# Kernel optimization log

Hardware: AMD Instinct MI355X
Metric: run time of the kernel (lower is better)

## Reference

```python
import jax, jax.numpy as jnp
import numpy as np

EPS = 1e-6


def setup_inputs() -> dict:
    key = jax.random.key(0)
    kq, kk, kv = jax.random.split(key, 3)
    B, H, S, D = 1, 16, 2048, 64
    q = jax.random.normal(kq, (B, H, S, D), dtype=jnp.float32)
    k = jax.random.normal(kk, (B, H, S, D), dtype=jnp.float32)
    v = jax.random.normal(kv, (B, H, S, D), dtype=jnp.float32)
    return {"q": q, "k": k, "v": v}


def reference(q, k, v):
    # Rebased linear attention: squared scaled QK score, causal mask,
    # normalized by running row-sum (not softmax).
    B, H, S, D = q.shape
    scale = D ** (-0.5)
    # [B,H,S,S] raw scores
    s = jnp.einsum("bhid,bhjd->bhij", q, k) * scale
    s2 = s * s
    causal = jnp.tril(jnp.ones((S, S), dtype=bool))  # k_idx <= q_idx
    s2 = jnp.where(causal, s2, jnp.zeros((), dtype=s2.dtype))
    z = jnp.sum(s2, axis=-1)  # [B,H,S]
    o = jnp.einsum("bhij,bhjd->bhid", s2, v)
    return o / (z[..., None] + EPS)
```

## Files before the change

### kernel.cpp

```cpp
#include <hip/hip_runtime.h>

typedef __attribute__((ext_vector_type(8))) short bf16x8;
typedef __attribute__((ext_vector_type(16))) float f32x16;

#define SLEN 2048
#define DDIM 64
#define NH 16
#define KEPS 1e-6f
#define TILE_B 16384
#define PSTR 72

__device__ __forceinline__ short f2bf(float x) {
    unsigned u = __float_as_uint(x);
    unsigned r = (u + 0x7FFFu + ((u >> 16) & 1u)) >> 16;
    return (short)r;
}
__device__ __forceinline__ unsigned cvtpk(float lo, float hi) {
    unsigned r;
    asm("v_cvt_pk_bf16_f32 %0, %1, %2" : "=v"(r) : "v"(lo), "v"(hi));
    return r;
}
__device__ __forceinline__ f32x16 mfma32x32(bf16x8 a, bf16x8 b, f32x16 c) {
    return __builtin_amdgcn_mfma_f32_32x32x16_bf16(a, b, c, 0, 0, 0);
}
__device__ __forceinline__ void gload16(const void* g, void* l) {
    __builtin_amdgcn_global_load_lds(
        (const __attribute__((address_space(1))) unsigned*)g,
        (__attribute__((address_space(3))) unsigned*)l, 16, 0, 0);
}

__global__ void __launch_bounds__(256) prep_kernel(
    const float* __restrict__ K, const float* __restrict__ V, char* __restrict__ WS)
{
    __shared__ short vt[64 * PSTR];
    const int b  = blockIdx.x;
    const int h  = b >> 5;
    const int kt = b & 31;
    const int t  = threadIdx.x;
    const int j  = t >> 2;
    const int ks = t & 3;
    const int c16 = ks * 16;

    char* chunk = WS + (size_t)b * TILE_B;

    {
        const float* src = K + ((size_t)h * SLEN + kt * 64 + j) * DDIM + c16;
        float4 a = ((const float4*)src)[0], bb = ((const float4*)src)[1];
        float4 c = ((const float4*)src)[2], d = ((const float4*)src)[3];
        uint4 lo = make_uint4(cvtpk(a.x,a.y), cvtpk(a.z,a.w), cvtpk(bb.x,bb.y), cvtpk(bb.z,bb.w));
        uint4 hi = make_uint4(cvtpk(c.x,c.y), cvtpk(c.z,c.w), cvtpk(d.x,d.y), cvtpk(d.z,d.w));
        *(uint4*)(chunk + ((size_t)((ks*2+0)*64 + j)) * 16) = lo;
        *(uint4*)(chunk + ((size_t)((ks*2+1)*64 + j)) * 16) = hi;
    }
    {
        const float* src = V + ((size_t)h * SLEN + kt * 64 + j) * DDIM + c16;
        float4 a = ((const float4*)src)[0], bb = ((const float4*)src)[1];
        float4 c = ((const float4*)src)[2], d = ((const float4*)src)[3];
        float f[16] = {a.x,a.y,a.z,a.w, bb.x,bb.y,bb.z,bb.w, c.x,c.y,c.z,c.w, d.x,d.y,d.z,d.w};
#pragma unroll
        for (int q = 0; q < 16; ++q)
            vt[(c16 + q) * PSTR + j] = f2bf(f[q]);
    }
    __syncthreads();
    {
        const int d  = t >> 2;
        const int jc = (t & 3) * 16;
        uint4 lo = *(const uint4*)&vt[d * PSTR + jc];
        uint4 hi = *(const uint4*)&vt[d * PSTR + jc + 8];
        char* vbase = chunk + 8192;
        *(uint4*)(vbase + (size_t)(((jc >> 4) * 2 + 0) * 64 + d) * 16) = lo;
        *(uint4*)(vbase + (size_t)(((jc >> 4) * 2 + 1) * 64 + d) * 16) = hi;
    }
}

template<bool WSP>
__device__ __forceinline__ void attn_body(
    const float* __restrict__ Q, const void* __restrict__ s1,
    const void* __restrict__ s2, float* __restrict__ O)
{
    __shared__ __align__(16) char smem[2][2][TILE_B];

    const int bid   = blockIdx.x;
    const int xcd   = bid & 7;
    const int r     = bid >> 3;
    const int h     = xcd | ((r & 1) << 3);
    const int u     = r >> 1;
    const int pg    = u & 15;
    const int halfb = u >> 4;

    const int tid  = threadIdx.x;
    const int w    = tid >> 6;
    const int lane = tid & 63;
    const int il   = lane & 31;
    const int hi   = lane >> 5;
    const int p    = w >> 2;
    const int qsel = (w >> 1) & 1;
    const int jb   = w & 1;

    const int grp   = qsel ? (31 - pg) : pg;
    const int q0    = grp * 64 + halfb * 32;
    const int ktmax = grp;
    const int ktstg = 31 - pg;

    const float* __restrict__ Qh = Q + (size_t)h * SLEN * DDIM;
    float* __restrict__ Oh = O + (size_t)h * SLEN * DDIM;

    bf16x8 qf[4];
#pragma unroll
    for (int ks = 0; ks < 4; ++ks) {
        const float* src = Qh + (size_t)(q0 + il) * DDIM + ks * 16 + hi * 8;
        float4 a = *reinterpret_cast<const float4*>(src);
        float4 b = *reinterpret_cast<const float4*>(src + 4);
        uint4 uq = make_uint4(cvtpk(a.x, a.y), cvtpk(a.z, a.w),
                              cvtpk(b.x, b.y), cvtpk(b.z, b.w));
        qf[ks] = *reinterpret_cast<bf16x8*>(&uq);
    }

    f32x16 oacc0, oacc1;
#pragma unroll
    for (int rr = 0; rr < 16; ++rr) { oacc0[rr] = 0.f; oacc1[rr] = 0.f; }
    float zacc = 0.f;

    const int wv = w & 3;
    const char* WSh = (const char*)s1 + (size_t)h * 32 * TILE_B;
    const int t255 = tid & 255;
    const int kr = t255 >> 2, kks = t255 & 3;
    const int vj0 = (t255 & 15) * 4, vd0 = (t255 >> 4) * 4;
    const float* Kf = (const float*)s1;
    const float* Vf = (const float*)s2;
    float4 kv[4], vv[4];

    auto stage_async = [&](int buf, int kt) {
        const char* g = WSh + (size_t)kt * TILE_B + wv * 4096 + lane * 16;
        char* l = &smem[p][buf][wv * 4096];
        gload16(g,        l);
        gload16(g + 1024, l + 1024);
        gload16(g + 2048, l + 2048);
        gload16(g + 3072, l + 3072);
    };
    auto issue_loads = [&](int kt) {
        const float* ks = Kf + ((size_t)h * SLEN + kt * 64 + kr) * DDIM + kks * 16;
#pragma unroll
        for (int i = 0; i < 4; ++i) kv[i] = reinterpret_cast<const float4*>(ks)[i];
#pragma unroll
        for (int rr = 0; rr < 4; ++rr)
            vv[rr] = *reinterpret_cast<const float4*>(
                Vf + ((size_t)h * SLEN + kt * 64 + vj0 + rr) * DDIM + vd0);
    };
    auto write_lds = [&](int buf) {
        char* kd = &smem[p][buf][0];
        uint4 lo = make_uint4(cvtpk(kv[0].x,kv[0].y), cvtpk(kv[0].z,kv[0].w),
                              cvtpk(kv[1].x,kv[1].y), cvtpk(kv[1].z,kv[1].w));
        uint4 hii = make_uint4(cvtpk(kv[2].x,kv[2].y), cvtpk(kv[2].z,kv[2].w),
                               cvtpk(kv[3].x,kv[3].y), cvtpk(kv[3].z,kv[3].w));
        *(uint4*)(kd + (size_t)((kks*2+0)*64 + kr) * 16) = lo;
        *(uint4*)(kd + (size_t)((kks*2+1)*64 + kr) * 16) = hii;
        char* vd = &smem[p][buf][8192];
        const int cv  = ((vj0 >> 4) * 2) + ((vj0 >> 3) & 1);
        const int tof = vj0 & 7;
#pragma unroll
        for (int c = 0; c < 4; ++c) {
            uint2 pk = make_uint2(
                cvtpk(((const float*)&vv[0])[c], ((const float*)&vv[1])[c]),
                cvtpk(((const float*)&vv[2])[c], ((const float*)&vv[3])[c]));
            *(uint2*)(vd + (size_t)(cv * 64 + vd0 + c) * 16 + tof * 2) = pk;
        }
    };

    const int T = (ktstg >> 1) + 1;

    if (WSP) { stage_async(0, p); }
    else     { issue_loads(p); write_lds(0); }
    __syncthreads();

    for (int t = 0; t < T; ++t) {
        const int kt  = 2 * t + p;
        const int nxt = kt + 2;
        const int cur = t & 1;

        if (nxt <= ktstg) { if (WSP) stage_async(cur ^ 1, nxt); else issue_loads(nxt); }

        if (kt <= ktmax && !(kt == ktmax && jb > halfb)) {
            const bool tri = (kt == ktmax) && (jb == halfb);
            const short* kp = (const short*)&smem[p][cur][0];
            const short* vp = (const short*)&smem[p][cur][8192];
            __builtin_amdgcn_s_setprio(1);
            f32x16 s;
#pragma unroll
            for (int rr = 0; rr < 16; ++rr) s[rr] = 0.f;
#pragma unroll
            for (int ks = 0; ks < 4; ++ks) {
                bf16x8 kf = *reinterpret_cast<const bf16x8*>(
                    kp + (size_t)((ks*2+hi)*64 + jb*32 + il) * 8);
                s = mfma32x32(kf, qf[ks], s);
            }
#pragma unroll
            for (int rr = 0; rr < 16; ++rr) {
                float x = s[rr];
                x = x * x * 0.015625f;
                if (tri) {
                    int jl = (rr & 3) + 8 * (rr >> 2) + 4 * hi;
                    if (jl > il) x = 0.f;
                }
                s[rr] = x;
                zacc += x;
            }
#pragma unroll
            for (int s16 = 0; s16 < 2; ++s16) {
                unsigned X  = cvtpk(s[8*s16+0], s[8*s16+1]);
                unsigned Xp = cvtpk(s[8*s16+2], s[8*s16+3]);
                unsigned Y  = cvtpk(s[8*s16+4], s[8*s16+5]);
                unsigned Yp = cvtpk(s[8*s16+6], s[8*s16+7]);
                asm("v_permlane32_swap_b32 %0, %1" : "+v"(X), "+v"(Y));
                asm("v_permlane32_swap_b32 %0, %1" : "+v"(Xp), "+v"(Yp));
                uint4 aw = make_uint4(X, Xp, Y, Yp);
                bf16x8 pf = *reinterpret_cast<bf16x8*>(&aw);
                {
                    bf16x8 vf = *reinterpret_cast<const bf16x8*>(
                        vp + (size_t)(((jb*2+s16)*2+hi)*64 + 0*32 + il) * 8);
                    oacc0 = mfma32x32(pf, vf, oacc0);
                }
                {
                    bf16x8 vf = *reinterpret_cast<const bf16x8*>(
                        vp + (size_t)(((jb*2+s16)*2+hi)*64 + 1*32 + il) * 8);
                    oacc1 = mfma32x32(pf, vf, oacc1);
                }
            }
            __builtin_amdgcn_s_setprio(0);
        }

        if (!WSP && nxt <= ktstg) write_lds(cur ^ 1);
        __syncthreads();
    }

    zacc += __shfl_xor(zacc, 32);
    float* red = (float*)smem;
    const int slot = p * 2 + jb;
    if (slot != 0) {
        float* rr_ = red + (size_t)((((slot - 1) * 2 + qsel) * 64 + lane) * 33);
#pragma unroll
        for (int rr = 0; rr < 16; ++rr) { rr_[rr] = oacc0[rr]; rr_[16 + rr] = oacc1[rr]; }
        rr_[32] = zacc;
    }
    __syncthreads();
    if (slot == 0) {
#pragma unroll
        for (int pp = 1; pp < 4; ++pp) {
            const float* rr_ = red + (size_t)((((pp - 1) * 2 + qsel) * 64 + lane) * 33);
#pragma unroll
            for (int rr = 0; rr < 16; ++rr) { oacc0[rr] += rr_[rr]; oacc1[rr] += rr_[16 + rr]; }
            zacc += rr_[32];
        }
        const float invl = 1.f / (zacc + KEPS);
#pragma unroll
        for (int rr = 0; rr < 16; ++rr) {
            const int rl = (rr & 3) + 8 * (rr >> 2) + 4 * hi;
            const float inv = __shfl(invl, rl);
            Oh[(size_t)(q0 + rl) * DDIM + il]      = oacc0[rr] * inv;
            Oh[(size_t)(q0 + rl) * DDIM + 32 + il] = oacc1[rr] * inv;
        }
    }
}

__global__ void __launch_bounds__(512, 4) attn_ws(
    const float* __restrict__ Q, const char* __restrict__ WS, float* __restrict__ O)
{
    attn_body<true>(Q, WS, nullptr, O);
}
__global__ void __launch_bounds__(512, 4) attn_fp32(
    const float* __restrict__ Q, const float* __restrict__ K,
    const float* __restrict__ V, float* __restrict__ O)
{
    attn_body<false>(Q, K, V, O);
}

extern "C" void kernel_launch(void* const* d_in, const int* in_sizes, int n_in,
                              void* d_out, int out_size, void* d_ws, size_t ws_size,
                              hipStream_t stream) {
    const float* q = (const float*)d_in[0];
    const float* k = (const float*)d_in[1];
    const float* v = (const float*)d_in[2];
    float* o = (float*)d_out;

    const size_t need = (size_t)NH * 32 * TILE_B;
    if (ws_size >= need) {
        char* ws = (char*)d_ws;
        hipLaunchKernelGGL(prep_kernel, dim3(NH * 32), dim3(256), 0, stream, k, v, ws);
        hipLaunchKernelGGL(attn_ws, dim3(512), dim3(512), 0, stream, q, ws, o);
    } else {
        hipLaunchKernelGGL(attn_fp32, dim3(512), dim3(512), 0, stream, q, k, v, o);
    }
}
```

Baseline: 35.75 us.

## Drop LDS staging; load prepacked K/V fragments directly from global into registers

The attention kernel no longer stages K/V tiles through double-buffered shared memory with async global-to-LDS loads and per-iteration barriers. Each wave now reads its MFMA operand fragments straight from the pre-swizzled workspace, prefetching the next K fragments in registers. Work is split so each wave owns one 32-query half, one key sub-block and alternating key tiles, with a reduction across four waves at the end. This removes the barriers and LDS traffic, but relies on L2/cache reuse because several waves re-read the same tiles from global memory.

```diff
diff --git a/kernel.cpp b/kernel.cpp
--- a/kernel.cpp
+++ b/kernel.cpp
@@ -22,11 +22,6 @@
 }
 __device__ __forceinline__ f32x16 mfma32x32(bf16x8 a, bf16x8 b, f32x16 c) {
     return __builtin_amdgcn_mfma_f32_32x32x16_bf16(a, b, c, 0, 0, 0);
-}
-__device__ __forceinline__ void gload16(const void* g, void* l) {
-    __builtin_amdgcn_global_load_lds(
-        (const __attribute__((address_space(1))) unsigned*)g,
-        (__attribute__((address_space(3))) unsigned*)l, 16, 0, 0);
 }
 
 __global__ void __launch_bounds__(256) prep_kernel(
@@ -73,37 +68,33 @@
     }
 }
 
-template<bool WSP>
-__device__ __forceinline__ void attn_body(
-    const float* __restrict__ Q, const void* __restrict__ s1,
-    const void* __restrict__ s2, float* __restrict__ O)
+__global__ void __launch_bounds__(512, 4) attn_main(
+    const float* __restrict__ Q, const char* __restrict__ WS, float* __restrict__ O)
 {
-    __shared__ __align__(16) char smem[2][2][TILE_B];
-
-    const int bid   = blockIdx.x;
-    const int xcd   = bid & 7;
-    const int r     = bid >> 3;
-    const int h     = xcd | ((r & 1) << 3);
-    const int u     = r >> 1;
-    const int pg    = u & 15;
-    const int halfb = u >> 4;
+    __shared__ float red[2][3][64][33];
+
+    const int bid = blockIdx.x;
+    const int xcd = bid & 7;
+    const int m   = bid >> 3;
+    const int h   = xcd | ((m & 1) << 3);
+    const int c   = m >> 1;
 
     const int tid  = threadIdx.x;
     const int w    = tid >> 6;
     const int lane = tid & 63;
     const int il   = lane & 31;
     const int hi   = lane >> 5;
-    const int p    = w >> 2;
-    const int qsel = (w >> 1) & 1;
-    const int jb   = w & 1;
-
-    const int grp   = qsel ? (31 - pg) : pg;
-    const int q0    = grp * 64 + halfb * 32;
-    const int ktmax = grp;
-    const int ktstg = 31 - pg;
+    const int msel = w >> 2;
+    const int jb   = (w >> 1) & 1;
+    const int e    = w & 1;
+
+    const int g    = msel ? (31 - c) : c;
+    const int half = msel;
+    const int q0   = g * 64 + half * 32;
 
     const float* __restrict__ Qh = Q + (size_t)h * SLEN * DDIM;
     float* __restrict__ Oh = O + (size_t)h * SLEN * DDIM;
+    const char* __restrict__ WSh = WS + (size_t)h * 32 * TILE_B;
 
     bf16x8 qf[4];
 #pragma unroll
@@ -121,79 +112,43 @@
     for (int rr = 0; rr < 16; ++rr) { oacc0[rr] = 0.f; oacc1[rr] = 0.f; }
     float zacc = 0.f;
 
-    const int wv = w & 3;
-    const char* WSh = (const char*)s1 + (size_t)h * 32 * TILE_B;
-    const int t255 = tid & 255;
-    const int kr = t255 >> 2, kks = t255 & 3;
-    const int vj0 = (t255 & 15) * 4, vd0 = (t255 >> 4) * 4;
-    const float* Kf = (const float*)s1;
-    const float* Vf = (const float*)s2;
-    float4 kv[4], vv[4];
-
-    auto stage_async = [&](int buf, int kt) {
-        const char* g = WSh + (size_t)kt * TILE_B + wv * 4096 + lane * 16;
-        char* l = &smem[p][buf][wv * 4096];
-        gload16(g,        l);
-        gload16(g + 1024, l + 1024);
-        gload16(g + 2048, l + 2048);
-        gload16(g + 3072, l + 3072);
-    };
-    auto issue_loads = [&](int kt) {
-        const float* ks = Kf + ((size_t)h * SLEN + kt * 64 + kr) * DDIM + kks * 16;
-#pragma unroll
-        for (int i = 0; i < 4; ++i) kv[i] = reinterpret_cast<const float4*>(ks)[i];
-#pragma unroll
-        for (int rr = 0; rr < 4; ++rr)
-            vv[rr] = *reinterpret_cast<const float4*>(
-                Vf + ((size_t)h * SLEN + kt * 64 + vj0 + rr) * DDIM + vd0);
-    };
-    auto write_lds = [&](int buf) {
-        char* kd = &smem[p][buf][0];
-        uint4 lo = make_uint4(cvtpk(kv[0].x,kv[0].y), cvtpk(kv[0].z,kv[0].w),
-                              cvtpk(kv[1].x,kv[1].y), cvtpk(kv[1].z,kv[1].w));
-        uint4 hii = make_uint4(cvtpk(kv[2].x,kv[2].y), cvtpk(kv[2].z,kv[2].w),
-                               cvtpk(kv[3].x,kv[3].y), cvtpk(kv[3].z,kv[3].w));
-        *(uint4*)(kd + (size_t)((kks*2+0)*64 + kr) * 16) = lo;
-        *(uint4*)(kd + (size_t)((kks*2+1)*64 + kr) * 16) = hii;
-        char* vd = &smem[p][buf][8192];
-        const int cv  = ((vj0 >> 4) * 2) + ((vj0 >> 3) & 1);
-        const int tof = vj0 & 7;
-#pragma unroll
-        for (int c = 0; c < 4; ++c) {
-            uint2 pk = make_uint2(
-                cvtpk(((const float*)&vv[0])[c], ((const float*)&vv[1])[c]),
-                cvtpk(((const float*)&vv[2])[c], ((const float*)&vv[3])[c]));
-            *(uint2*)(vd + (size_t)(cv * 64 + vd0 + c) * 16 + tof * 2) = pk;
-        }
-    };
-
-    const int T = (ktstg >> 1) + 1;
-
-    if (WSP) { stage_async(0, p); }
-    else     { issue_loads(p); write_lds(0); }
-    __syncthreads();
-
-    for (int t = 0; t < T; ++t) {
-        const int kt  = 2 * t + p;
-        const int nxt = kt + 2;
-        const int cur = t & 1;
-
-        if (nxt <= ktstg) { if (WSP) stage_async(cur ^ 1, nxt); else issue_loads(nxt); }
-
-        if (kt <= ktmax && !(kt == ktmax && jb > halfb)) {
-            const bool tri = (kt == ktmax) && (jb == halfb);
-            const short* kp = (const short*)&smem[p][cur][0];
-            const short* vp = (const short*)&smem[p][cur][8192];
-            __builtin_amdgcn_s_setprio(1);
+    const int koff = (hi * 64 + jb * 32 + il) * 16;
+    const int voff = 8192 + ((jb * 2 * 2 + hi) * 64 + il) * 16;
+
+    const int ktend = g - ((jb > half) ? 1 : 0);
+
+    if (e <= ktend) {
+        const char* kb = WSh + (size_t)e * TILE_B + koff;
+        bf16x8 kf0 = *(const bf16x8*)(kb);
+        bf16x8 kf1 = *(const bf16x8*)(kb + 2048);
+        bf16x8 kf2 = *(const bf16x8*)(kb + 4096);
+        bf16x8 kf3 = *(const bf16x8*)(kb + 6144);
+
+        for (int kt = e; kt <= ktend; kt += 2) {
+            const char* tb = WSh + (size_t)kt * TILE_B;
+            const char* vb = tb + voff;
+            bf16x8 v00 = *(const bf16x8*)(vb);
+            bf16x8 v01 = *(const bf16x8*)(vb + 512);
+            bf16x8 v10 = *(const bf16x8*)(vb + 2048);
+            bf16x8 v11 = *(const bf16x8*)(vb + 2560);
+
             f32x16 s;
 #pragma unroll
             for (int rr = 0; rr < 16; ++rr) s[rr] = 0.f;
-#pragma unroll
-            for (int ks = 0; ks < 4; ++ks) {
-                bf16x8 kf = *reinterpret_cast<const bf16x8*>(
-                    kp + (size_t)((ks*2+hi)*64 + jb*32 + il) * 8);
-                s = mfma32x32(kf, qf[ks], s);
-            }
+            s = mfma32x32(kf0, qf[0], s);
+            s = mfma32x32(kf1, qf[1], s);
+            s = mfma32x32(kf2, qf[2], s);
+            s = mfma32x32(kf3, qf[3], s);
+
+            if (kt + 2 <= ktend) {
+                const char* nb = WSh + (size_t)(kt + 2) * TILE_B + koff;
+                kf0 = *(const bf16x8*)(nb);
+                kf1 = *(const bf16x8*)(nb + 2048);
+                kf2 = *(const bf16x8*)(nb + 4096);
+                kf3 = *(const bf16x8*)(nb + 6144);
+            }
+
+            const bool tri = (kt == g) && (jb == half);
 #pragma unroll
             for (int rr = 0; rr < 16; ++rr) {
                 float x = s[rr];
@@ -203,53 +158,58 @@
                     if (jl > il) x = 0.f;
                 }
                 s[rr] = x;
-                zacc += x;
-            }
-#pragma unroll
-            for (int s16 = 0; s16 < 2; ++s16) {
-                unsigned X  = cvtpk(s[8*s16+0], s[8*s16+1]);
-                unsigned Xp = cvtpk(s[8*s16+2], s[8*s16+3]);
-                unsigned Y  = cvtpk(s[8*s16+4], s[8*s16+5]);
-                unsigned Yp = cvtpk(s[8*s16+6], s[8*s16+7]);
+            }
+            {
+                float a0 = (s[0] + s[1]) + (s[2] + s[3]);
+                float a1 = (s[4] + s[5]) + (s[6] + s[7]);
+                float a2 = (s[8] + s[9]) + (s[10] + s[11]);
+                float a3 = (s[12] + s[13]) + (s[14] + s[15]);
+                zacc += (a0 + a1) + (a2 + a3);
+            }
+
+            {
+                unsigned X  = cvtpk(s[0], s[1]);
+                unsigned Xp = cvtpk(s[2], s[3]);
+                unsigned Y  = cvtpk(s[4], s[5]);
+                unsigned Yp = cvtpk(s[6], s[7]);
                 asm("v_permlane32_swap_b32 %0, %1" : "+v"(X), "+v"(Y));
                 asm("v_permlane32_swap_b32 %0, %1" : "+v"(Xp), "+v"(Yp));
                 uint4 aw = make_uint4(X, Xp, Y, Yp);
                 bf16x8 pf = *reinterpret_cast<bf16x8*>(&aw);
-                {
-                    bf16x8 vf = *reinterpret_cast<const bf16x8*>(
-                        vp + (size_t)(((jb*2+s16)*2+hi)*64 + 0*32 + il) * 8);
-                    oacc0 = mfma32x32(pf, vf, oacc0);
-                }
-                {
-                    bf16x8 vf = *reinterpret_cast<const bf16x8*>(
-                        vp + (size_t)(((jb*2+s16)*2+hi)*64 + 1*32 + il) * 8);
-                    oacc1 = mfma32x32(pf, vf, oacc1);
-                }
-            }
-            __builtin_amdgcn_s_setprio(0);
-        }
-
-        if (!WSP && nxt <= ktstg) write_lds(cur ^ 1);
-        __syncthreads();
+                oacc0 = mfma32x32(pf, v00, oacc0);
+                oacc1 = mfma32x32(pf, v01, oacc1);
+            }
+            {
+                unsigned X  = cvtpk(s[8],  s[9]);
+                unsigned Xp = cvtpk(s[10], s[11]);
+                unsigned Y  = cvtpk(s[12], s[13]);
+                unsigned Yp = cvtpk(s[14], s[15]);
+                asm("v_permlane32_swap_b32 %0, %1" : "+v"(X), "+v"(Y));
+                asm("v_permlane32_swap_b32 %0, %1" : "+v"(Xp), "+v"(Yp));
+                uint4 aw = make_uint4(X, Xp, Y, Yp);
+                bf16x8 pf = *reinterpret_cast<bf16x8*>(&aw);
+                oacc0 = mfma32x32(pf, v10, oacc0);
+                oacc1 = mfma32x32(pf, v11, oacc1);
+            }
+        }
     }
 
     zacc += __shfl_xor(zacc, 32);
-    float* red = (float*)smem;
-    const int slot = p * 2 + jb;
-    if (slot != 0) {
-        float* rr_ = red + (size_t)((((slot - 1) * 2 + qsel) * 64 + lane) * 33);
-#pragma unroll
-        for (int rr = 0; rr < 16; ++rr) { rr_[rr] = oacc0[rr]; rr_[16 + rr] = oacc1[rr]; }
-        rr_[32] = zacc;
+    const int sw = w & 3;
+    if (sw != 0) {
+        float* r = &red[msel][sw - 1][lane][0];
+#pragma unroll
+        for (int rr = 0; rr < 16; ++rr) { r[rr] = oacc0[rr]; r[16 + rr] = oacc1[rr]; }
+        r[32] = zacc;
     }
     __syncthreads();
-    if (slot == 0) {
-#pragma unroll
-        for (int pp = 1; pp < 4; ++pp) {
-            const float* rr_ = red + (size_t)((((pp - 1) * 2 + qsel) * 64 + lane) * 33);
-#pragma unroll
-            for (int rr = 0; rr < 16; ++rr) { oacc0[rr] += rr_[rr]; oacc1[rr] += rr_[16 + rr]; }
-            zacc += rr_[32];
+    if (sw == 0) {
+#pragma unroll
+        for (int pp = 0; pp < 3; ++pp) {
+            const float* r = &red[msel][pp][lane][0];
+#pragma unroll
+            for (int rr = 0; rr < 16; ++rr) { oacc0[rr] += r[rr]; oacc1[rr] += r[16 + rr]; }
+            zacc += r[32];
         }
         const float invl = 1.f / (zacc + KEPS);
 #pragma unroll
@@ -262,16 +222,130 @@
     }
 }
 
-__global__ void __launch_bounds__(512, 4) attn_ws(
-    const float* __restrict__ Q, const char* __restrict__ WS, float* __restrict__ O)
-{
-    attn_body<true>(Q, WS, nullptr, O);
-}
 __global__ void __launch_bounds__(512, 4) attn_fp32(
     const float* __restrict__ Q, const float* __restrict__ K,
     const float* __restrict__ V, float* __restrict__ O)
 {
-    attn_body<false>(Q, K, V, O);
+    __shared__ float red[2][3][64][33];
+
+    const int bid = blockIdx.x;
+    const int xcd = bid & 7;
+    const int m   = bid >> 3;
+    const int h   = xcd | ((m & 1) << 3);
+    const int c   = m >> 1;
+
+    const int tid  = threadIdx.x;
+    const int w    = tid >> 6;
+    const int lane = tid & 63;
+    const int il   = lane & 31;
+    const int hi   = lane >> 5;
+    const int msel = w >> 2;
+    const int jb   = (w >> 1) & 1;
+    const int e    = w & 1;
+
+    const int g    = msel ? (31 - c) : c;
+    const int half = msel;
+    const int q0   = g * 64 + half * 32;
+
+    const float* Qh = Q + (size_t)h * SLEN * DDIM;
+    const float* Kh = K + (size_t)h * SLEN * DDIM;
+    const float* Vh = V + (size_t)h * SLEN * DDIM;
+    float* Oh = O + (size_t)h * SLEN * DDIM;
+
+    bf16x8 qf[4];
+#pragma unroll
+    for (int ks = 0; ks < 4; ++ks) {
+        const float* src = Qh + (size_t)(q0 + il) * DDIM + ks * 16 + hi * 8;
+        float4 a = *reinterpret_cast<const float4*>(src);
+        float4 b = *reinterpret_cast<const float4*>(src + 4);
+        uint4 uq = make_uint4(cvtpk(a.x, a.y), cvtpk(a.z, a.w),
+                              cvtpk(b.x, b.y), cvtpk(b.z, b.w));
+        qf[ks] = *reinterpret_cast<bf16x8*>(&uq);
+    }
+
+    f32x16 oacc0, oacc1;
+#pragma unroll
+    for (int rr = 0; rr < 16; ++rr) { oacc0[rr] = 0.f; oacc1[rr] = 0.f; }
+    float zacc = 0.f;
+
+    const int ktend = g - ((jb > half) ? 1 : 0);
+
+    for (int kt = e; kt <= ktend; kt += 2) {
+        f32x16 s;
+#pragma unroll
+        for (int rr = 0; rr < 16; ++rr) s[rr] = 0.f;
+#pragma unroll
+        for (int ks = 0; ks < 4; ++ks) {
+            const float* src = Kh + (size_t)(kt * 64 + jb * 32 + il) * DDIM + ks * 16 + hi * 8;
+            float4 a = *reinterpret_cast<const float4*>(src);
+            float4 b = *reinterpret_cast<const float4*>(src + 4);
+            uint4 uk = make_uint4(cvtpk(a.x, a.y), cvtpk(a.z, a.w),
+                                  cvtpk(b.x, b.y), cvtpk(b.z, b.w));
+            s = mfma32x32(*reinterpret_cast<bf16x8*>(&uk), qf[ks], s);
+        }
+        const bool tri = (kt == g) && (jb == half);
+#pragma unroll
+        for (int rr = 0; rr < 16; ++rr) {
+            float x = s[rr];
+            x = x * x * 0.015625f;
+            if (tri) {
+                int jl = (rr & 3) + 8 * (rr >> 2) + 4 * hi;
+                if (jl > il) x = 0.f;
+            }
+            s[rr] = x;
+            zacc += x;
+        }
+#pragma unroll
+        for (int s16 = 0; s16 < 2; ++s16) {
+            unsigned X  = cvtpk(s[8*s16+0], s[8*s16+1]);
+            unsigned Xp = cvtpk(s[8*s16+2], s[8*s16+3]);
+            unsigned Y  = cvtpk(s[8*s16+4], s[8*s16+5]);
+            unsigned Yp = cvtpk(s[8*s16+6], s[8*s16+7]);
+            asm("v_permlane32_swap_b32 %0, %1" : "+v"(X), "+v"(Y));
+            asm("v_permlane32_swap_b32 %0, %1" : "+v"(Xp), "+v"(Yp));
+            uint4 aw = make_uint4(X, Xp, Y, Yp);
+            bf16x8 pf = *reinterpret_cast<bf16x8*>(&aw);
+#pragma unroll
+            for (int dt = 0; dt < 2; ++dt) {
+                float v8[8];
+#pragma unroll
+                for (int t = 0; t < 8; ++t)
+                    v8[t] = Vh[(size_t)(kt * 64 + (jb * 2 + s16) * 16 + hi * 8 + t) * DDIM + dt * 32 + il];
+                uint4 uv = make_uint4(cvtpk(v8[0], v8[1]), cvtpk(v8[2], v8[3]),
+                                      cvtpk(v8[4], v8[5]), cvtpk(v8[6], v8[7]));
+                bf16x8 vf = *reinterpret_cast<bf16x8*>(&uv);
+                if (dt == 0) oacc0 = mfma32x32(pf, vf, oacc0);
+                else         oacc1 = mfma32x32(pf, vf, oacc1);
+            }
+        }
+    }
+
+    zacc += __shfl_xor(zacc, 32);
+    const int sw = w & 3;
+    if (sw != 0) {
+        float* r = &red[msel][sw - 1][lane][0];
+#pragma unroll
+        for (int rr = 0; rr < 16; ++rr) { r[rr] = oacc0[rr]; r[16 + rr] = oacc1[rr]; }
+        r[32] = zacc;
+    }
+    __syncthreads();
+    if (sw == 0) {
+#pragma unroll
+        for (int pp = 0; pp < 3; ++pp) {
+            const float* r = &red[msel][pp][lane][0];
+#pragma unroll
+            for (int rr = 0; rr < 16; ++rr) { oacc0[rr] += r[rr]; oacc1[rr] += r[16 + rr]; }
+            zacc += r[32];
+        }
+        const float invl = 1.f / (zacc + KEPS);
+#pragma unroll
+        for (int rr = 0; rr < 16; ++rr) {
+            const int rl = (rr & 3) + 8 * (rr >> 2) + 4 * hi;
+            const float inv = __shfl(invl, rl);
+            Oh[(size_t)(q0 + rl) * DDIM + il]      = oacc0[rr] * inv;
+            Oh[(size_t)(q0 + rl) * DDIM + 32 + il] = oacc1[rr] * inv;
+        }
+    }
 }
 
 extern "C" void kernel_launch(void* const* d_in, const int* in_sizes, int n_in,
@@ -286,7 +360,7 @@
     if (ws_size >= need) {
         char* ws = (char*)d_ws;
         hipLaunchKernelGGL(prep_kernel, dim3(NH * 32), dim3(256), 0, stream, k, v, ws);
-        hipLaunchKernelGGL(attn_ws, dim3(512), dim3(512), 0, stream, q, ws, o);
+        hipLaunchKernelGGL(attn_main, dim3(512), dim3(512), 0, stream, q, ws, o);
     } else {
         hipLaunchKernelGGL(attn_fp32, dim3(512), dim3(512), 0, stream, q, k, v, o);
     }
```

Result: faster. 30.78 us (-13.9%).
